# Kernel optimization log

Measured on AMD Instinct MI355X. Metric: run time of the kernel, lower is better.

The kernel has to match this reference:

```python
import jax, jax.numpy as jnp
import numpy as np

H, DH = 16, 64          # num_heads, dim_head
DIM = 1024              # dim_ltn
EPS = 1e-5


def setup_inputs() -> dict:
    key = jax.random.key(0)
    ks = jax.random.split(key, 8)
    b, n_txt, t, m = 2, 2048, 4, 256
    text = jax.random.normal(ks[0], (b, n_txt, DIM), dtype=jnp.float32)
    image = jax.random.normal(ks[1], (b, t, m, DIM), dtype=jnp.float32)
    locations = jax.random.randint(ks[2], (b, n_txt), 0, 2)  # 0/1 media markers
    s = DIM ** -0.5
    Wq = jax.random.normal(ks[3], (DIM, H * DH), dtype=jnp.float32) * s
    Wkv = jax.random.normal(ks[4], (DIM, 2 * H * DH), dtype=jnp.float32) * s
    Wo = jax.random.normal(ks[5], (H * DH, DIM), dtype=jnp.float32) * s
    ln_gamma = jnp.ones((DIM,), dtype=jnp.float32)
    ln_beta = jnp.zeros((DIM,), dtype=jnp.float32)
    return {"text": text, "image": image, "locations": locations,
            "Wq": Wq, "Wkv": Wkv, "Wo": Wo,
            "ln_gamma": ln_gamma, "ln_beta": ln_beta}


def reference(text, image, locations, Wq, Wkv, Wo, ln_gamma, ln_beta):
    scale = DH ** -0.5
    b, t, m, d = image.shape
    # LayerNorm(text)
    mu = text.mean(-1, keepdims=True)
    var = ((text - mu) ** 2).mean(-1, keepdims=True)
    tn = (text - mu) / jnp.sqrt(var + EPS) * ln_gamma + ln_beta
    img = image.reshape(b, t * m, d)             # b (t m) d
    q = tn @ Wq                                  # b n (h dh)
    k, v = jnp.split(img @ Wkv, 2, axis=-1)      # each b tm (h dh)
    split_heads = lambda x: x.reshape(x.shape[0], x.shape[1], H, DH).transpose(0, 2, 1, 3)
    q, k, v = split_heads(q), split_heads(k), split_heads(v)
    attn = jnp.einsum('bhid,bhjd->bhij', q, k) * scale   # b h n (t m)
    txt_time = jnp.cumsum(locations, axis=-1)            # b n : media index per text token
    viz_time = jnp.repeat(jnp.arange(1, t + 1), m)       # (t m)
    # only_attend_to_immediate -> equality mask
    mask = txt_time[:, None, :, None] == viz_time[None, None, None, :]
    neg = -jnp.finfo(attn.dtype).max
    attn = jnp.where(mask, attn, neg)
    attn = jax.nn.softmax(attn, axis=-1)
    # zero attention for text tokens before any media (txt_time == 0)
    attn = jnp.where((txt_time == 0)[:, None, :, None], 0.0, attn)
    out = jnp.einsum('bhij,bhjd->bhid', attn, v)
    out = out.transpose(0, 2, 1, 3).reshape(b, -1, H * DH)
    return out @ Wo
```

## Files before the change

kernel.cpp:

```cpp
#include <hip/hip_runtime.h>

#define BATCH 2
#define NTXT  2048
#define TMED  4
#define MMED  256
#define TM    (TMED * MMED)
#define DIM   1024
#define NH    16
#define DHD   64
#define KVW   2048
#define RMAX  256
#define RT    32

typedef _Float16 f16x8 __attribute__((ext_vector_type(8)));
typedef float    f32x4 __attribute__((ext_vector_type(4)));

__global__ __launch_bounds__(1024) void k1_scan_ibar(
    const int* __restrict__ loc, const float* __restrict__ image,
    int* __restrict__ tt, int* __restrict__ seg, float* __restrict__ ibar,
    _Float16* __restrict__ img16) {
  __shared__ int buf[NTXT];
  __shared__ int s_start, s_end;
  const int idx = blockIdx.x;
  const int tid = threadIdx.x;
  if (idx < BATCH) {
    const int b = idx;
    if (tid == 0) { s_start = NTXT; s_end = NTXT; }
    buf[tid]        = loc[b * NTXT + tid];
    buf[tid + 1024] = loc[b * NTXT + tid + 1024];
    __syncthreads();
    for (int off = 1; off < NTXT; off <<= 1) {
      int a0 = (tid >= off) ? buf[tid - off] : 0;
      int a1 = buf[tid + 1024 - off];
      __syncthreads();
      buf[tid] += a0;
      buf[tid + 1024] += a1;
      __syncthreads();
    }
    const int v0 = buf[tid], v1 = buf[tid + 1024];
    tt[b * NTXT + tid]        = v0;
    tt[b * NTXT + tid + 1024] = v1;
    if (v0 >= 1) atomicMin(&s_start, tid);
    if (v0 >= 5) atomicMin(&s_end, tid);
    if (v1 >= 1) atomicMin(&s_start, tid + 1024);
    if (v1 >= 5) atomicMin(&s_end, tid + 1024);
    __syncthreads();
    if (tid == 0) {
      seg[b * 2]     = s_start;
      seg[b * 2 + 1] = s_end - s_start;
    }
  } else {
    const int j = idx - BATCH;
    const int b = j >> 3, rt = j & 7;
    const size_t base = (size_t)(b * TM + rt * 128) * DIM + tid;
    const float* p = image + base;
    _Float16* q = img16 + base;
    float s = 0.f;
#pragma unroll 4
    for (int r = 0; r < 128; r++) {
      const float v = p[(size_t)r * DIM];
      s += v;
      q[(size_t)r * DIM] = (_Float16)v;
    }
    atomicAdd(&ibar[b * DIM + tid], s * (1.0f / (float)TM));
  }
}

__global__ __launch_bounds__(256) void k2_prep(
    const float* __restrict__ Wkv, const float* __restrict__ text,
    const float* __restrict__ gamma, const float* __restrict__ beta,
    const int* __restrict__ seg, const float* __restrict__ ibar,
    _Float16* __restrict__ WkvT, float* __restrict__ tn,
    float* __restrict__ vbar) {
  __shared__ float tile[64][65];
  __shared__ float red[256];
  const int idx = blockIdx.x;
  const int tid = threadIdx.x;
  if (idx < 512) {
    const int k0 = (idx & 15) * 64, n0 = (idx >> 4) * 64;
    const int r = tid >> 4, c4 = (tid & 15) * 4;
#pragma unroll
    for (int i = 0; i < 4; i++) {
      const float4 v = *reinterpret_cast<const float4*>(
          Wkv + (size_t)(k0 + r + i * 16) * KVW + n0 + c4);
      tile[r + i * 16][c4 + 0] = v.x; tile[r + i * 16][c4 + 1] = v.y;
      tile[r + i * 16][c4 + 2] = v.z; tile[r + i * 16][c4 + 3] = v.w;
    }
    __syncthreads();
#pragma unroll
    for (int it = 0; it < 2; it++) {
      const int chunk = it * 256 + tid;
      const int n = chunk >> 3, kc = (chunk & 7) * 8;
      f16x8 h;
#pragma unroll
      for (int j = 0; j < 8; j++) h[j] = (_Float16)tile[kc + j][n];
      *reinterpret_cast<f16x8*>(WkvT + (size_t)(n0 + n) * DIM + k0 + kc) = h;
    }
  } else if (idx < 576) {
    const int j = idx - 512;
    const int b = j >> 5, rt = j & 31;
    const int i0 = seg[b * 2];
    const int cnt = min(seg[b * 2 + 1], RMAX);
    for (int r = rt; r < cnt; r += RT) {
      const float* xrow = text + (size_t)(b * NTXT + i0 + r) * DIM;
      float x[4];
      float s = 0.f;
#pragma unroll
      for (int u = 0; u < 4; u++) { x[u] = xrow[tid + 256 * u]; s += x[u]; }
      red[tid] = s; __syncthreads();
      for (int st = 128; st > 0; st >>= 1) {
        if (tid < st) red[tid] += red[tid + st];
        __syncthreads();
      }
      const float mu = red[0] * (1.0f / DIM); __syncthreads();
      float vs = 0.f;
#pragma unroll
      for (int u = 0; u < 4; u++) { float d = x[u] - mu; vs += d * d; }
      red[tid] = vs; __syncthreads();
      for (int st = 128; st > 0; st >>= 1) {
        if (tid < st) red[tid] += red[tid + st];
        __syncthreads();
      }
      const float rstd = rsqrtf(red[0] * (1.0f / DIM) + 1e-5f); __syncthreads();
      float* trow = tn + (size_t)(b * RMAX + r) * DIM;
#pragma unroll
      for (int u = 0; u < 4; u++) {
        const int c = tid + 256 * u;
        trow[c] = (x[u] - mu) * rstd * gamma[c] + beta[c];
      }
      __syncthreads();
    }
  } else {
    const int j = idx - 576;
    const int b = j >> 5, et = (j >> 3) & 3, cc = j & 7;
    const int e = et * 256 + tid;
    const int c0 = cc * 128;
    if (tid < 128) red[tid] = ibar[b * DIM + c0 + tid];
    __syncthreads();
    float s = 0.f;
    for (int c = 0; c < 128; c++)
      s += red[c] * Wkv[(size_t)(c0 + c) * KVW + DIM + e];
    atomicAdd(&vbar[b * DIM + e], s);
  }
}

__global__ __launch_bounds__(512) void k3_gemm_qproj_obar(
    const _Float16* __restrict__ img16, const _Float16* __restrict__ WkvT,
    const float* __restrict__ Wq, const float* __restrict__ Wo,
    const float* __restrict__ tn, const float* __restrict__ vbar,
    const int* __restrict__ seg, _Float16* __restrict__ kv16,
    float* __restrict__ qbuf, float* __restrict__ obar) {
  __shared__ char smem[16384];
  const int idx = blockIdx.x;
  const int tid = threadIdx.x;
  if (idx < 256) {
    _Float16* As = (_Float16*)smem;
    _Float16* Bs = As + 128 * 32;
    const int lane = tid & 63, wid = tid >> 6;
    const int wm = wid & 3, wn = wid >> 2;
    const int row0 = (idx >> 4) * 128, col0 = (idx & 15) * 128;
    const int srow = tid >> 2, skc = (tid & 3) * 8;
    const int frow = lane & 15, fq = lane >> 4;
    f32x4 acc[2][4] = {};
    for (int k0 = 0; k0 < DIM; k0 += 32) {
      const f16x8 av = *reinterpret_cast<const f16x8*>(
          img16 + (size_t)(row0 + srow) * DIM + k0 + skc);
      const f16x8 bv = *reinterpret_cast<const f16x8*>(
          WkvT + (size_t)(col0 + srow) * DIM + k0 + skc);
      __syncthreads();
      *reinterpret_cast<f16x8*>(As + tid * 8) = av;
      *reinterpret_cast<f16x8*>(Bs + tid * 8) = bv;
      __syncthreads();
      f16x8 af[2], bf[4];
#pragma unroll
      for (int mt = 0; mt < 2; mt++)
        af[mt] = *reinterpret_cast<const f16x8*>(
            As + (wm * 32 + mt * 16 + frow) * 32 + fq * 8);
#pragma unroll
      for (int nt = 0; nt < 4; nt++)
        bf[nt] = *reinterpret_cast<const f16x8*>(
            Bs + (wn * 64 + nt * 16 + frow) * 32 + fq * 8);
#pragma unroll
      for (int mt = 0; mt < 2; mt++)
#pragma unroll
        for (int nt = 0; nt < 4; nt++)
          acc[mt][nt] = __builtin_amdgcn_mfma_f32_16x16x32_f16(
              af[mt], bf[nt], acc[mt][nt], 0, 0, 0);
    }
#pragma unroll
    for (int mt = 0; mt < 2; mt++)
#pragma unroll
      for (int nt = 0; nt < 4; nt++) {
        const int col = col0 + wn * 64 + nt * 16 + frow;
#pragma unroll
        for (int r = 0; r < 4; r++) {
          const int row = row0 + wm * 32 + mt * 16 + fq * 4 + r;
          kv16[(size_t)row * KVW + col] = (_Float16)acc[mt][nt][r];
        }
      }
  } else if (idx < 320) {
    float* tn_s = (float*)smem;
    const int j = idx - 256;
    const int b = j >> 5, nt = (j >> 2) & 7, cc = j & 3;
    const int n0 = nt * 128, c0 = cc * 256;
    const int n = tid & 127, cs = tid >> 7;
    const int cnt = min(seg[b * 2 + 1], RMAX);
    for (int r0 = 0; r0 < cnt; r0 += 8) {
      const int rows = min(8, cnt - r0);
      for (int i = tid; i < 8 * 256; i += 512) {
        const int r = i >> 8, c = i & 255;
        tn_s[i] = (r < rows) ? tn[(size_t)(b * RMAX + r0 + r) * DIM + c0 + c]
                             : 0.f;
      }
      __syncthreads();
      float acc[8] = {};
      for (int ci = 0; ci < 64; ci++) {
        const int c = cs * 64 + ci;
        const float w = Wq[(size_t)(c0 + c) * DIM + n0 + n];
#pragma unroll
        for (int rr = 0; rr < 8; rr++) acc[rr] += tn_s[rr * 256 + c] * w;
      }
      for (int rr = 0; rr < rows; rr++)
        atomicAdd(&qbuf[(size_t)(b * RMAX + r0 + rr) * DIM + n0 + n], acc[rr]);
      __syncthreads();
    }
  } else {
    float* vb_s = (float*)smem;
    const int j = idx - 320;
    const int b = j >> 4, et = (j >> 3) & 1, cc = j & 7;
    const int e = et * 512 + tid;
    const int c0 = cc * 128;
    if (tid < 128) vb_s[tid] = vbar[b * DIM + c0 + tid];
    __syncthreads();
    float s = 0.f;
    for (int c = 0; c < 128; c++)
      s += vb_s[c] * Wo[(size_t)(c0 + c) * DIM + e];
    atomicAdd(&obar[b * DIM + e], s);
  }
}

__global__ __launch_bounds__(256) void k4_fill_attn(
    const float* __restrict__ text, const _Float16* __restrict__ kv16,
    const float* __restrict__ Wq, const float* __restrict__ Wo,
    const float* __restrict__ gamma, const float* __restrict__ beta,
    const int* __restrict__ tt, const int* __restrict__ seg,
    const float* __restrict__ obar, const float* __restrict__ qbuf,
    float* __restrict__ oacc, float* __restrict__ out) {
  __shared__ float red[256];
  __shared__ float pbuf[256];
  const int idx = blockIdx.x;
  const int tid = threadIdx.x;
  if (idx < BATCH * NTXT) {
    const int b = idx >> 11;
    const int i = idx & (NTXT - 1);
    const int t = tt[b * NTXT + i];
    float* orow = out + (size_t)(b * NTXT + i) * DIM;
    if (t == 0) {
      for (int c = tid; c < DIM; c += 256) orow[c] = 0.f;
      return;
    }
    if (t > TMED) {
      const float* ob = obar + b * DIM;
      for (int c = tid; c < DIM; c += 256) orow[c] = ob[c];
      return;
    }
    if (i - seg[b * 2] < RMAX) return;
    __shared__ float tns[DIM];
    __shared__ float qrow[DIM];
    __shared__ float oaccs[DIM];
    const float* xrow = text + (size_t)(b * NTXT + i) * DIM;
    float x[4];
    float s = 0.f;
#pragma unroll
    for (int u = 0; u < 4; u++) { x[u] = xrow[tid + 256 * u]; s += x[u]; }
    red[tid] = s; __syncthreads();
    for (int st = 128; st > 0; st >>= 1) {
      if (tid < st) red[tid] += red[tid + st];
      __syncthreads();
    }
    const float mu = red[0] * (1.0f / DIM); __syncthreads();
    float vs = 0.f;
#pragma unroll
    for (int u = 0; u < 4; u++) { float d = x[u] - mu; vs += d * d; }
    red[tid] = vs; __syncthreads();
    for (int st = 128; st > 0; st >>= 1) {
      if (tid < st) red[tid] += red[tid + st];
      __syncthreads();
    }
    const float rstd = rsqrtf(red[0] * (1.0f / DIM) + 1e-5f); __syncthreads();
#pragma unroll
    for (int u = 0; u < 4; u++) {
      const int c = tid + 256 * u;
      tns[c] = (x[u] - mu) * rstd * gamma[c] + beta[c];
    }
    __syncthreads();
    {
      float qa[4] = {0.f, 0.f, 0.f, 0.f};
      for (int c = 0; c < DIM; c++) {
        const float tv = tns[c];
        const float* w = Wq + (size_t)c * DIM + tid;
#pragma unroll
        for (int u = 0; u < 4; u++) qa[u] += tv * w[256 * u];
      }
#pragma unroll
      for (int u = 0; u < 4; u++) qrow[tid + 256 * u] = qa[u];
    }
    __syncthreads();
    const size_t kvrow0 = (size_t)(b * TM + (t - 1) * MMED) * KVW;
    const int d0 = tid & 63, g = tid >> 6;
    for (int h = 0; h < NH; h++) {
      const _Float16* krow = kv16 + kvrow0 + (size_t)tid * KVW + h * DHD;
      float sc = 0.f;
#pragma unroll
      for (int d = 0; d < DHD; d++) sc += qrow[h * DHD + d] * (float)krow[d];
      sc *= 0.125f;
      red[tid] = sc; __syncthreads();
      for (int st = 128; st > 0; st >>= 1) {
        if (tid < st) red[tid] = fmaxf(red[tid], red[tid + st]);
        __syncthreads();
      }
      const float mx = red[0]; __syncthreads();
      const float e = __expf(sc - mx);
      red[tid] = e; __syncthreads();
      for (int st = 128; st > 0; st >>= 1) {
        if (tid < st) red[tid] += red[tid + st];
        __syncthreads();
      }
      const float inv = 1.0f / red[0]; __syncthreads();
      pbuf[tid] = e * inv; __syncthreads();
      const _Float16* vbase = kv16 + kvrow0 + (size_t)(g * 64) * KVW + DIM + h * DHD + d0;
      float a = 0.f;
#pragma unroll 8
      for (int jj = 0; jj < 64; jj++) a += pbuf[g * 64 + jj] * (float)vbase[(size_t)jj * KVW];
      red[tid] = a; __syncthreads();
      if (tid < 64)
        oaccs[h * DHD + tid] = red[tid] + red[64 + tid] + red[128 + tid] + red[192 + tid];
      __syncthreads();
    }
    float oa[4] = {0.f, 0.f, 0.f, 0.f};
    for (int c = 0; c < DIM; c++) {
      const float ov = oaccs[c];
      const float* w = Wo + (size_t)c * DIM + tid;
#pragma unroll
      for (int u = 0; u < 4; u++) oa[u] += ov * w[256 * u];
    }
#pragma unroll
    for (int u = 0; u < 4; u++) orow[tid + 256 * u] = oa[u];
  } else {
    __shared__ float qs[DHD];
    const int j = idx - BATCH * NTXT;
    const int h = j & 15, rt = (j >> 4) & 31, b = j >> 9;
    const int i0 = seg[b * 2];
    const int cnt = min(seg[b * 2 + 1], RMAX);
    const int d0 = tid & 63, g = tid >> 6;
    for (int r = rt; r < cnt; r += RT) {
      const int i = i0 + r;
      const int t = tt[b * NTXT + i];
      if (tid < 64) qs[tid] = qbuf[(size_t)(b * RMAX + r) * DIM + h * DHD + tid];
      __syncthreads();
      const size_t kvrow0 = (size_t)(b * TM + (t - 1) * MMED) * KVW;
      const _Float16* krow = kv16 + kvrow0 + (size_t)tid * KVW + h * DHD;
      float sc = 0.f;
#pragma unroll
      for (int d = 0; d < DHD; d += 8) {
        const f16x8 kk = *reinterpret_cast<const f16x8*>(krow + d);
#pragma unroll
        for (int u = 0; u < 8; u++) sc += qs[d + u] * (float)kk[u];
      }
      sc *= 0.125f;
      red[tid] = sc; __syncthreads();
      for (int st = 128; st > 0; st >>= 1) {
        if (tid < st) red[tid] = fmaxf(red[tid], red[tid + st]);
        __syncthreads();
      }
      const float mx = red[0]; __syncthreads();
      const float e = __expf(sc - mx);
      red[tid] = e; __syncthreads();
      for (int st = 128; st > 0; st >>= 1) {
        if (tid < st) red[tid] += red[tid + st];
        __syncthreads();
      }
      const float inv = 1.0f / red[0]; __syncthreads();
      pbuf[tid] = e * inv; __syncthreads();
      const _Float16* vbase = kv16 + kvrow0 + (size_t)(g * 64) * KVW + DIM + h * DHD + d0;
      float a = 0.f;
#pragma unroll 8
      for (int jj = 0; jj < 64; jj++) a += pbuf[g * 64 + jj] * (float)vbase[(size_t)jj * KVW];
      red[tid] = a; __syncthreads();
      if (tid < 64)
        oacc[(size_t)(b * RMAX + r) * DIM + h * DHD + tid] =
            red[tid] + red[64 + tid] + red[128 + tid] + red[192 + tid];
      __syncthreads();
    }
  }
}

__global__ __launch_bounds__(256) void k5_oproj(
    const float* __restrict__ oacc, const float* __restrict__ Wo,
    const int* __restrict__ seg, float* __restrict__ out) {
  const int ct = blockIdx.x;
  const int rt = blockIdx.y;
  const int b = blockIdx.z;
  const int i0 = seg[b * 2];
  const int cnt = min(seg[b * 2 + 1], RMAX);
  const int tid = threadIdx.x;
  const int d0 = tid & 63, g = tid >> 6;
  __shared__ float op[4][64];
  for (int r = rt; r < cnt; r += RT) {
    const float* arow = oacc + (size_t)(b * RMAX + r) * DIM;
    const float* wo = Wo + (size_t)(g * 256) * DIM + ct * 64 + d0;
    float s = 0.f;
    for (int c = 0; c < 256; c++) s += arow[g * 256 + c] * wo[(size_t)c * DIM];
    op[g][d0] = s; __syncthreads();
    if (tid < 64)
      out[(size_t)(b * NTXT + i0 + r) * DIM + ct * 64 + tid] =
          op[0][tid] + op[1][tid] + op[2][tid] + op[3][tid];
    __syncthreads();
  }
}

extern "C" void kernel_launch(void* const* d_in, const int* in_sizes, int n_in,
                              void* d_out, int out_size, void* d_ws, size_t ws_size,
                              hipStream_t stream) {
  const float* text  = (const float*)d_in[0];
  const float* image = (const float*)d_in[1];
  const int*   loc   = (const int*)d_in[2];
  const float* Wq    = (const float*)d_in[3];
  const float* Wkv   = (const float*)d_in[4];
  const float* Wo    = (const float*)d_in[5];
  const float* gamma = (const float*)d_in[6];
  const float* beta  = (const float*)d_in[7];
  float* out = (float*)d_out;

  _Float16* kv16  = (_Float16*)d_ws;
  _Float16* WkvT  = kv16 + (size_t)BATCH * TM * KVW;
  float*    oacc  = (float*)WkvT;
  _Float16* img16 = WkvT + (size_t)KVW * DIM;
  float*    tn    = (float*)(img16 + (size_t)BATCH * TM * DIM);
  float*    qbuf  = tn + (size_t)BATCH * RMAX * DIM;
  float*    ibar  = qbuf + (size_t)BATCH * RMAX * DIM;
  float*    vbar  = ibar + BATCH * DIM;
  float*    obar  = vbar + BATCH * DIM;
  int*      tt    = (int*)(obar + BATCH * DIM);
  int*      seg   = tt + BATCH * NTXT;

  hipMemsetAsync(qbuf, 0,
                 ((size_t)BATCH * RMAX * DIM + 3 * BATCH * DIM) * sizeof(float),
                 stream);
  k1_scan_ibar<<<BATCH + 16, 1024, 0, stream>>>(loc, image, tt, seg, ibar, img16);
  k2_prep<<<640, 256, 0, stream>>>(Wkv, text, gamma, beta, seg, ibar,
                                   WkvT, tn, vbar);
  k3_gemm_qproj_obar<<<352, 512, 0, stream>>>(img16, WkvT, Wq, Wo, tn, vbar,
                                              seg, kv16, qbuf, obar);
  k4_fill_attn<<<BATCH * NTXT + NH * RT * BATCH, 256, 0, stream>>>(
      text, kv16, Wq, Wo, gamma, beta, tt, seg, obar, qbuf, oacc, out);
  k5_oproj<<<dim3(16, RT, BATCH), 256, 0, stream>>>(oacc, Wo, seg, out);
}
```

Baseline: 159.6 us.

## Move Wkv transpose into k1, widen image conversion, use direct-to-LDS loads in KV GEMM

The Wkv fp16 transpose moves from k2 into k1, and the image fp32-to-fp16 conversion is split across 256 blocks that write partial column sums. k2 now reduces those partials, which replaces the atomic ibar accumulation. The KV GEMM drops to 256 threads per block, with each wave computing a 64x64 tile. Its tiles are staged with global_load_lds direct-to-LDS loads, and a block-index swizzle improves L2 locality. The aim is more parallelism in the conversion and less register staging in the GEMM. The cost is larger per-wave accumulator use and a serial 128-way partial reduction in k2.

Result: slower. 169.1 us (+5.9%).

```diff
diff --git a/kernel.cpp b/kernel.cpp
--- a/kernel.cpp
+++ b/kernel.cpp
@@ -15,12 +15,19 @@
 typedef _Float16 f16x8 __attribute__((ext_vector_type(8)));
 typedef float    f32x4 __attribute__((ext_vector_type(4)));
 
-__global__ __launch_bounds__(1024) void k1_scan_ibar(
+#define GLOAD_LDS16(g, l)                                                  \
+  __builtin_amdgcn_global_load_lds(                                        \
+      (const __attribute__((address_space(1))) unsigned int*)(g),          \
+      (__attribute__((address_space(3))) unsigned int*)(l), 16, 0, 0)
+
+__global__ __launch_bounds__(1024) void k1_scan_cvt_tr(
     const int* __restrict__ loc, const float* __restrict__ image,
-    int* __restrict__ tt, int* __restrict__ seg, float* __restrict__ ibar,
-    _Float16* __restrict__ img16) {
+    const float* __restrict__ Wkv, int* __restrict__ tt, int* __restrict__ seg,
+    float* __restrict__ ipart, _Float16* __restrict__ img16,
+    _Float16* __restrict__ WkvT) {
   __shared__ int buf[NTXT];
   __shared__ int s_start, s_end;
+  __shared__ float tile[64][65];
   const int idx = blockIdx.x;
   const int tid = threadIdx.x;
   if (idx < BATCH) {
@@ -49,56 +56,49 @@
       seg[b * 2]     = s_start;
       seg[b * 2 + 1] = s_end - s_start;
     }
-  } else {
+  } else if (idx < BATCH + 256) {
     const int j = idx - BATCH;
-    const int b = j >> 3, rt = j & 7;
-    const size_t base = (size_t)(b * TM + rt * 128) * DIM + tid;
+    const int b = j >> 7, rt = j & 127;
+    const size_t base = (size_t)(b * TM + rt * 8) * DIM + tid;
     const float* p = image + base;
     _Float16* q = img16 + base;
     float s = 0.f;
-#pragma unroll 4
-    for (int r = 0; r < 128; r++) {
+#pragma unroll
+    for (int r = 0; r < 8; r++) {
       const float v = p[(size_t)r * DIM];
       s += v;
       q[(size_t)r * DIM] = (_Float16)v;
     }
-    atomicAdd(&ibar[b * DIM + tid], s * (1.0f / (float)TM));
+    ipart[(size_t)(b * 128 + rt) * DIM + tid] = s;
+  } else {
+    const int j2 = idx - BATCH - 256;
+    const int k0 = (j2 & 15) * 64, n0 = (j2 >> 4) * 64;
+    const int r = tid >> 4, c4 = (tid & 15) * 4;
+    const float4 v = *reinterpret_cast<const float4*>(
+        Wkv + (size_t)(k0 + r) * KVW + n0 + c4);
+    tile[r][c4 + 0] = v.x; tile[r][c4 + 1] = v.y;
+    tile[r][c4 + 2] = v.z; tile[r][c4 + 3] = v.w;
+    __syncthreads();
+    if (tid < 512) {
+      const int n = tid >> 3, kc = (tid & 7) * 8;
+      f16x8 h;
+#pragma unroll
+      for (int u = 0; u < 8; u++) h[u] = (_Float16)tile[kc + u][n];
+      *reinterpret_cast<f16x8*>(WkvT + (size_t)(n0 + n) * DIM + k0 + kc) = h;
+    }
   }
 }
 
 __global__ __launch_bounds__(256) void k2_prep(
     const float* __restrict__ Wkv, const float* __restrict__ text,
     const float* __restrict__ gamma, const float* __restrict__ beta,
-    const int* __restrict__ seg, const float* __restrict__ ibar,
-    _Float16* __restrict__ WkvT, float* __restrict__ tn,
-    float* __restrict__ vbar) {
-  __shared__ float tile[64][65];
+    const int* __restrict__ seg, const float* __restrict__ ipart,
+    float* __restrict__ tn, float* __restrict__ vbar) {
   __shared__ float red[256];
   const int idx = blockIdx.x;
   const int tid = threadIdx.x;
-  if (idx < 512) {
-    const int k0 = (idx & 15) * 64, n0 = (idx >> 4) * 64;
-    const int r = tid >> 4, c4 = (tid & 15) * 4;
-#pragma unroll
-    for (int i = 0; i < 4; i++) {
-      const float4 v = *reinterpret_cast<const float4*>(
-          Wkv + (size_t)(k0 + r + i * 16) * KVW + n0 + c4);
-      tile[r + i * 16][c4 + 0] = v.x; tile[r + i * 16][c4 + 1] = v.y;
-      tile[r + i * 16][c4 + 2] = v.z; tile[r + i * 16][c4 + 3] = v.w;
-    }
-    __syncthreads();
-#pragma unroll
-    for (int it = 0; it < 2; it++) {
-      const int chunk = it * 256 + tid;
-      const int n = chunk >> 3, kc = (chunk & 7) * 8;
-      f16x8 h;
-#pragma unroll
-      for (int j = 0; j < 8; j++) h[j] = (_Float16)tile[kc + j][n];
-      *reinterpret_cast<f16x8*>(WkvT + (size_t)(n0 + n) * DIM + k0 + kc) = h;
-    }
-  } else if (idx < 576) {
-    const int j = idx - 512;
-    const int b = j >> 5, rt = j & 31;
+  if (idx < 64) {
+    const int b = idx >> 5, rt = idx & 31;
     const int i0 = seg[b * 2];
     const int cnt = min(seg[b * 2 + 1], RMAX);
     for (int r = rt; r < cnt; r += RT) {
@@ -131,11 +131,16 @@
       __syncthreads();
     }
   } else {
-    const int j = idx - 576;
+    const int j = idx - 64;
     const int b = j >> 5, et = (j >> 3) & 3, cc = j & 7;
     const int e = et * 256 + tid;
     const int c0 = cc * 128;
-    if (tid < 128) red[tid] = ibar[b * DIM + c0 + tid];
+    if (tid < 128) {
+      float s = 0.f;
+      for (int p = 0; p < 128; p++)
+        s += ipart[(size_t)(b * 128 + p) * DIM + c0 + tid];
+      red[tid] = s * (1.0f / (float)TM);
+    }
     __syncthreads();
     float s = 0.f;
     for (int c = 0; c < 128; c++)
@@ -144,57 +149,61 @@
   }
 }
 
-__global__ __launch_bounds__(512) void k3_gemm_qproj_obar(
+__global__ __launch_bounds__(256) void k3_gemm_qproj_obar(
     const _Float16* __restrict__ img16, const _Float16* __restrict__ WkvT,
     const float* __restrict__ Wq, const float* __restrict__ Wo,
     const float* __restrict__ tn, const float* __restrict__ vbar,
     const int* __restrict__ seg, _Float16* __restrict__ kv16,
     float* __restrict__ qbuf, float* __restrict__ obar) {
-  __shared__ char smem[16384];
+  __shared__ __align__(16) char smem[16384];
   const int idx = blockIdx.x;
   const int tid = threadIdx.x;
   if (idx < 256) {
     _Float16* As = (_Float16*)smem;
     _Float16* Bs = As + 128 * 32;
+    const int swz = (idx & 7) * 32 + (idx >> 3);
     const int lane = tid & 63, wid = tid >> 6;
-    const int wm = wid & 3, wn = wid >> 2;
-    const int row0 = (idx >> 4) * 128, col0 = (idx & 15) * 128;
-    const int srow = tid >> 2, skc = (tid & 3) * 8;
+    const int wm = wid & 1, wn = wid >> 1;
+    const int row0 = (swz >> 4) * 128, col0 = (swz & 15) * 128;
     const int frow = lane & 15, fq = lane >> 4;
-    f32x4 acc[2][4] = {};
+    const int srow = lane >> 2, skc = (lane & 3) * 8;
+    f32x4 acc[4][4] = {};
     for (int k0 = 0; k0 < DIM; k0 += 32) {
-      const f16x8 av = *reinterpret_cast<const f16x8*>(
-          img16 + (size_t)(row0 + srow) * DIM + k0 + skc);
-      const f16x8 bv = *reinterpret_cast<const f16x8*>(
-          WkvT + (size_t)(col0 + srow) * DIM + k0 + skc);
-      __syncthreads();
-      *reinterpret_cast<f16x8*>(As + tid * 8) = av;
-      *reinterpret_cast<f16x8*>(Bs + tid * 8) = bv;
-      __syncthreads();
-      f16x8 af[2], bf[4];
-#pragma unroll
-      for (int mt = 0; mt < 2; mt++)
+      __syncthreads();
+#pragma unroll
+      for (int i = 0; i < 2; i++) {
+        const int ci = wid * 2 + i;
+        const int r = ci * 16 + srow;
+        GLOAD_LDS16(img16 + (size_t)(row0 + r) * DIM + k0 + skc,
+                    As + ci * 512);
+        GLOAD_LDS16(WkvT + (size_t)(col0 + r) * DIM + k0 + skc,
+                    Bs + ci * 512);
+      }
+      __syncthreads();
+      f16x8 af[4], bf[4];
+#pragma unroll
+      for (int mt = 0; mt < 4; mt++)
         af[mt] = *reinterpret_cast<const f16x8*>(
-            As + (wm * 32 + mt * 16 + frow) * 32 + fq * 8);
+            As + (wm * 64 + mt * 16 + frow) * 32 + fq * 8);
 #pragma unroll
       for (int nt = 0; nt < 4; nt++)
         bf[nt] = *reinterpret_cast<const f16x8*>(
             Bs + (wn * 64 + nt * 16 + frow) * 32 + fq * 8);
 #pragma unroll
-      for (int mt = 0; mt < 2; mt++)
+      for (int mt = 0; mt < 4; mt++)
 #pragma unroll
         for (int nt = 0; nt < 4; nt++)
           acc[mt][nt] = __builtin_amdgcn_mfma_f32_16x16x32_f16(
               af[mt], bf[nt], acc[mt][nt], 0, 0, 0);
     }
 #pragma unroll
-    for (int mt = 0; mt < 2; mt++)
+    for (int mt = 0; mt < 4; mt++)
 #pragma unroll
       for (int nt = 0; nt < 4; nt++) {
         const int col = col0 + wn * 64 + nt * 16 + frow;
 #pragma unroll
         for (int r = 0; r < 4; r++) {
-          const int row = row0 + wm * 32 + mt * 16 + fq * 4 + r;
+          const int row = row0 + wm * 64 + mt * 16 + fq * 4 + r;
           kv16[(size_t)row * KVW + col] = (_Float16)acc[mt][nt][r];
         }
       }
@@ -207,15 +216,15 @@
     const int cnt = min(seg[b * 2 + 1], RMAX);
     for (int r0 = 0; r0 < cnt; r0 += 8) {
       const int rows = min(8, cnt - r0);
-      for (int i = tid; i < 8 * 256; i += 512) {
+      for (int i = tid; i < 8 * 256; i += 256) {
         const int r = i >> 8, c = i & 255;
         tn_s[i] = (r < rows) ? tn[(size_t)(b * RMAX + r0 + r) * DIM + c0 + c]
                              : 0.f;
       }
       __syncthreads();
       float acc[8] = {};
-      for (int ci = 0; ci < 64; ci++) {
-        const int c = cs * 64 + ci;
+      for (int ci = 0; ci < 128; ci++) {
+        const int c = cs * 128 + ci;
         const float w = Wq[(size_t)(c0 + c) * DIM + n0 + n];
 #pragma unroll
         for (int rr = 0; rr < 8; rr++) acc[rr] += tn_s[rr * 256 + c] * w;
@@ -227,8 +236,8 @@
   } else {
     float* vb_s = (float*)smem;
     const int j = idx - 320;
-    const int b = j >> 4, et = (j >> 3) & 1, cc = j & 7;
-    const int e = et * 512 + tid;
+    const int b = j >> 5, et = (j >> 3) & 3, cc = j & 7;
+    const int e = et * 256 + tid;
     const int c0 = cc * 128;
     if (tid < 128) vb_s[tid] = vbar[b * DIM + c0 + tid];
     __syncthreads();
@@ -438,19 +447,19 @@
   _Float16* img16 = WkvT + (size_t)KVW * DIM;
   float*    tn    = (float*)(img16 + (size_t)BATCH * TM * DIM);
   float*    qbuf  = tn + (size_t)BATCH * RMAX * DIM;
-  float*    ibar  = qbuf + (size_t)BATCH * RMAX * DIM;
-  float*    vbar  = ibar + BATCH * DIM;
+  float*    vbar  = qbuf + (size_t)BATCH * RMAX * DIM;
   float*    obar  = vbar + BATCH * DIM;
   int*      tt    = (int*)(obar + BATCH * DIM);
   int*      seg   = tt + BATCH * NTXT;
+  float*    ipart = (float*)(seg + 8);
 
   hipMemsetAsync(qbuf, 0,
-                 ((size_t)BATCH * RMAX * DIM + 3 * BATCH * DIM) * sizeof(float),
+                 ((size_t)BATCH * RMAX * DIM + 2 * BATCH * DIM) * sizeof(float),
                  stream);
-  k1_scan_ibar<<<BATCH + 16, 1024, 0, stream>>>(loc, image, tt, seg, ibar, img16);
-  k2_prep<<<640, 256, 0, stream>>>(Wkv, text, gamma, beta, seg, ibar,
-                                   WkvT, tn, vbar);
-  k3_gemm_qproj_obar<<<352, 512, 0, stream>>>(img16, WkvT, Wq, Wo, tn, vbar,
+  k1_scan_cvt_tr<<<BATCH + 256 + 512, 1024, 0, stream>>>(
+      loc, image, Wkv, tt, seg, ipart, img16, WkvT);
+  k2_prep<<<128, 256, 0, stream>>>(Wkv, text, gamma, beta, seg, ipart, tn, vbar);
+  k3_gemm_qproj_obar<<<384, 256, 0, stream>>>(img16, WkvT, Wq, Wo, tn, vbar,
                                               seg, kv16, qbuf, obar);
   k4_fill_attn<<<BATCH * NTXT + NH * RT * BATCH, 256, 0, stream>>>(
       text, kv16, Wq, Wo, gamma, beta, tt, seg, obar, qbuf, oacc, out);
```
